# Kernel tuning notes

Hardware: AMD Instinct MI355X
Metric: run time of the kernel (lower is better)

## Reference

```python
import jax, jax.numpy as jnp
import numpy as np

N_NODES = 50000
N_EDGES = 1600000
IN_CH = 128
HID = 128
OUT_CH = 2
N_GRAPHS = 512
N_HID_LAYERS = 5  # first 5 SAGEConv+BN+ReLU blocks; 6th conv has no BN/act
EPS = 1e-5


def setup_inputs() -> dict:
    key = jax.random.key(0)
    ks = jax.random.split(key, 13)
    x = jax.random.normal(ks[0], (N_NODES, IN_CH), jnp.float32)
    edge_index = jax.random.randint(ks[1], (2, N_EDGES), 0, N_NODES)
    batch = jnp.sort(jax.random.randint(ks[2], (N_NODES,), 0, N_GRAPHS))
    s = 1.0 / np.sqrt(HID)
    # SAGEConv params for the 5 hidden layers (in==hid==128 so they stack)
    Wl = jax.random.normal(ks[3], (N_HID_LAYERS, HID, HID), jnp.float32) * s  # lin_l (neighbors)
    Wr = jax.random.normal(ks[4], (N_HID_LAYERS, HID, HID), jnp.float32) * s  # lin_r (root)
    b = jax.random.normal(ks[5], (N_HID_LAYERS, HID), jnp.float32) * s
    # BatchNorm (eval mode: running stats + affine)
    gamma = 1.0 + 0.1 * jax.random.normal(ks[6], (N_HID_LAYERS, HID), jnp.float32)
    beta = 0.1 * jax.random.normal(ks[7], (N_HID_LAYERS, HID), jnp.float32)
    rmean = 0.1 * jax.random.normal(ks[8], (N_HID_LAYERS, HID), jnp.float32)
    rvar = 0.5 + jax.random.uniform(ks[9], (N_HID_LAYERS, HID), dtype=jnp.float32)
    # final SAGEConv: hid -> out
    Wl_out = jax.random.normal(ks[10], (HID, OUT_CH), jnp.float32) * s
    Wr_out = jax.random.normal(ks[11], (HID, OUT_CH), jnp.float32) * s
    b_out = jax.random.normal(ks[12], (OUT_CH,), jnp.float32) * s
    return dict(x=x, Wl=Wl, Wr=Wr, b=b, gamma=gamma, beta=beta, rmean=rmean,
                rvar=rvar, Wl_out=Wl_out, Wr_out=Wr_out, b_out=b_out,
                edge_index=edge_index, batch=batch)


def reference(x, Wl, Wr, b, gamma, beta, rmean, rvar, Wl_out, Wr_out, b_out,
              edge_index, batch):
    src, dst = edge_index[0], edge_index[1]
    # in-degree for mean aggregation (shared across all layers)
    deg = jax.ops.segment_sum(jnp.ones((src.shape[0],), x.dtype), dst,
                              num_segments=N_NODES)
    inv_deg = (1.0 / jnp.maximum(deg, 1.0))[:, None]  # [N,1]

    def sage(h, Wl_, Wr_, b_):
        # PyG SAGEConv: lin_l(mean_{j in N(i)} x_j) + lin_r(x_i)
        agg = jax.ops.segment_sum(h[src], dst, num_segments=N_NODES) * inv_deg
        return agg @ Wl_ + h @ Wr_ + b_

    h = x
    for l in range(N_HID_LAYERS):
        h = sage(h, Wl[l], Wr[l], b[l])
        # BatchNorm1d in eval mode: affine with running stats
        h = (h - rmean[l]) * (gamma[l] * jax.lax.rsqrt(rvar[l] + EPS)) + beta[l]
        h = jax.nn.relu(h)
        # F.dropout(p=0.2, training=False) is identity in eval
    h = sage(h, Wl_out, Wr_out, b_out)  # [N, OUT_CH]
    # global_mean_pool over graphs
    gsum = jax.ops.segment_sum(h, batch, num_segments=N_GRAPHS)
    gcnt = jax.ops.segment_sum(jnp.ones((h.shape[0],), h.dtype), batch,
                               num_segments=N_GRAPHS)
    return gsum / jnp.maximum(gcnt, 1.0)[:, None]  # [N_GRAPHS, OUT_CH]
```

## Files before the change

### kernel.cpp

```cpp
#include <hip/hip_runtime.h>

#define HID 128
#define BN_EPS 1e-5f

typedef short bf16x8 __attribute__((ext_vector_type(8)));
typedef float f32x4 __attribute__((ext_vector_type(4)));

__device__ inline unsigned short f2b(float f) {
  unsigned int u = __float_as_uint(f);
  unsigned int r = (u + 0x7fffu + ((u >> 16) & 1u)) >> 16;
  return (unsigned short)r;
}
__device__ inline float bl(unsigned int v) { return __uint_as_float(v << 16); }
__device__ inline float bh(unsigned int v) { return __uint_as_float(v & 0xffff0000u); }


__global__ void k_bhist(const int* __restrict__ dst, int* __restrict__ bcnt, int e, int nb) {
  __shared__ int h[256];
  for (int i = threadIdx.x; i < 256; i += blockDim.x) h[i] = 0;
  __syncthreads();
  int stride = gridDim.x * blockDim.x;
  for (int i = blockIdx.x * blockDim.x + threadIdx.x; i < e; i += stride)
    atomicAdd(&h[dst[i] >> 8], 1);
  __syncthreads();
  for (int i = threadIdx.x; i < nb; i += blockDim.x)
    if (h[i]) atomicAdd(&bcnt[i], h[i]);
}

__global__ void k_bscan(const int* __restrict__ bcnt, int* __restrict__ base,
                        int* __restrict__ cur, int nb) {
  __shared__ int ws[4];
  int t = threadIdx.x;
  int v = (t < nb) ? bcnt[t] : 0;
  int lane = t & 63, wid = t >> 6;
  int x = v;
#pragma unroll
  for (int off = 1; off < 64; off <<= 1) {
    int y = __shfl_up(x, off, 64);
    if (lane >= off) x += y;
  }
  if (lane == 63) ws[wid] = x;
  __syncthreads();
  int add = 0;
  for (int w = 0; w < wid; ++w) add += ws[w];
  int incl = x + add;
  int excl = incl - v;
  if (t < nb) { base[t] = excl; cur[t] = excl; }
  if (t == nb - 1) base[nb] = incl;
}

__global__ void k_bscatter(const int* __restrict__ src, const int* __restrict__ dst,
                           int* __restrict__ cur, uint2* __restrict__ binned, int e) {
  __shared__ int bc[256];
  __shared__ int bo[256];
  int nchunk = (e + gridDim.x - 1) / gridDim.x;
  int c0 = blockIdx.x * nchunk;
  int c1 = min(c0 + nchunk, e);
  for (int i = threadIdx.x; i < 256; i += blockDim.x) bc[i] = 0;
  __syncthreads();
  for (int i = c0 + threadIdx.x; i < c1; i += blockDim.x)
    atomicAdd(&bc[dst[i] >> 8], 1);
  __syncthreads();
  for (int i = threadIdx.x; i < 256; i += blockDim.x) {
    int c = bc[i];
    bo[i] = c ? atomicAdd(&cur[i], c) : 0;
    bc[i] = 0;
  }
  __syncthreads();
  for (int i = c0 + threadIdx.x; i < c1; i += blockDim.x) {
    int d = dst[i];
    int b = d >> 8;
    int pos = bo[b] + atomicAdd(&bc[b], 1);
    binned[pos] = make_uint2((unsigned)src[i], (unsigned)d);
  }
}

__global__ __launch_bounds__(256) void k_bfill(
    const uint2* __restrict__ binned, const int* __restrict__ base,
    int* __restrict__ row_ptr, float* __restrict__ inv_deg,
    int* __restrict__ col, int n, int nb) {
  __shared__ int cnt[256];
  __shared__ int cur[256];
  __shared__ int ws[4];
  int b = blockIdx.x;
  int t = threadIdx.x;
  int n0 = b << 8;
  int e0 = base[b], e1 = base[b + 1];
  cnt[t] = 0;
  __syncthreads();
  for (int i = e0 + t; i < e1; i += 256)
    atomicAdd(&cnt[binned[i].y & 255], 1);
  __syncthreads();
  int v = cnt[t];
  int lane = t & 63, wid = t >> 6;
  int x = v;
#pragma unroll
  for (int off = 1; off < 64; off <<= 1) {
    int y = __shfl_up(x, off, 64);
    if (lane >= off) x += y;
  }
  if (lane == 63) ws[wid] = x;
  __syncthreads();
  int add = 0;
  for (int w = 0; w < wid; ++w) add += ws[w];
  int excl = x - v + add;
  int node = n0 + t;
  if (node < n) {
    row_ptr[node] = e0 + excl;
    inv_deg[node] = 1.0f / (float)max(v, 1);
  }
  cur[t] = e0 + excl;
  __syncthreads();
  for (int i = e0 + t; i < e1; i += 256) {
    uint2 pr = binned[i];
    int pos = atomicAdd(&cur[pr.y & 255], 1);
    col[pos] = (int)pr.x;
  }
  if (b == 0 && t == 0) row_ptr[n] = base[nb];
}


__global__ void k_prep(const float* __restrict__ x, unsigned short* __restrict__ xb,
                       const float* __restrict__ Wl, const float* __restrict__ Wr,
                       unsigned short* __restrict__ Wlt, unsigned short* __restrict__ Wrt,
                       const float* __restrict__ g, const float* __restrict__ be,
                       const float* __restrict__ rm, const float* __restrict__ rv,
                       float* __restrict__ sc, float* __restrict__ sh,
                       int n4, int wtot, int bn) {
  int i = blockIdx.x * blockDim.x + threadIdx.x;
  if (i < n4) {
    float4 v = ((const float4*)x)[i];
    unsigned int lo = (unsigned int)f2b(v.x) | ((unsigned int)f2b(v.y) << 16);
    unsigned int hi = (unsigned int)f2b(v.z) | ((unsigned int)f2b(v.w) << 16);
    ((uint2*)xb)[i] = make_uint2(lo, hi);
  } else if (i < n4 + wtot) {
    int j = i - n4;
    int mat = j >> 14, rem = j & 16383, nn = rem >> 7, kk = rem & 127;
    int sidx = (mat << 14) + (kk << 7) + nn;
    Wlt[j] = f2b(Wl[sidx]);
    Wrt[j] = f2b(Wr[sidx]);
  } else if (i < n4 + wtot + bn) {
    int j = i - n4 - wtot;
    float s = g[j] * rsqrtf(rv[j] + BN_EPS);
    sc[j] = s;
    sh[j] = be[j] - rm[j] * s;
  }
}


__global__ __launch_bounds__(256) void k_spmm_g(
    const unsigned short* __restrict__ hbsrc, const int* __restrict__ row_ptr,
    const int* __restrict__ col, const float* __restrict__ inv_deg,
    unsigned short* __restrict__ aggb, int n) {
  int node = blockIdx.x * 4 + (threadIdx.x >> 6);
  if (node >= n) return;
  int lane = threadIdx.x & 63;
  int slot = lane >> 4, c16 = lane & 15;
  int beg = row_ptr[node], end = row_ptr[node + 1];
  float a0 = 0, a1 = 0, a2 = 0, a3 = 0, a4 = 0, a5 = 0, a6 = 0, a7 = 0;
  const unsigned short* base = hbsrc + (c16 << 3);
  int e = beg;
  for (; e + 16 <= end; e += 16) {
    int s0 = col[e + slot];
    int s1 = col[e + 4 + slot];
    int s2 = col[e + 8 + slot];
    int s3 = col[e + 12 + slot];
    uint4 v0 = *(const uint4*)(base + ((size_t)s0 << 7));
    uint4 v1 = *(const uint4*)(base + ((size_t)s1 << 7));
    uint4 v2 = *(const uint4*)(base + ((size_t)s2 << 7));
    uint4 v3 = *(const uint4*)(base + ((size_t)s3 << 7));
    a0 += bl(v0.x); a1 += bh(v0.x); a2 += bl(v0.y); a3 += bh(v0.y);
    a4 += bl(v0.z); a5 += bh(v0.z); a6 += bl(v0.w); a7 += bh(v0.w);
    a0 += bl(v1.x); a1 += bh(v1.x); a2 += bl(v1.y); a3 += bh(v1.y);
    a4 += bl(v1.z); a5 += bh(v1.z); a6 += bl(v1.w); a7 += bh(v1.w);
    a0 += bl(v2.x); a1 += bh(v2.x); a2 += bl(v2.y); a3 += bh(v2.y);
    a4 += bl(v2.z); a5 += bh(v2.z); a6 += bl(v2.w); a7 += bh(v2.w);
    a0 += bl(v3.x); a1 += bh(v3.x); a2 += bl(v3.y); a3 += bh(v3.y);
    a4 += bl(v3.z); a5 += bh(v3.z); a6 += bl(v3.w); a7 += bh(v3.w);
  }
  for (; e < end; e += 4) {
    int idx = e + slot;
    if (idx < end) {
      int s = col[idx];
      uint4 v = *(const uint4*)(base + ((size_t)s << 7));
      a0 += bl(v.x); a1 += bh(v.x); a2 += bl(v.y); a3 += bh(v.y);
      a4 += bl(v.z); a5 += bh(v.z); a6 += bl(v.w); a7 += bh(v.w);
    }
  }
#pragma unroll
  for (int st = 16; st <= 32; st <<= 1) {
    a0 += __shfl_xor(a0, st); a1 += __shfl_xor(a1, st);
    a2 += __shfl_xor(a2, st); a3 += __shfl_xor(a3, st);
    a4 += __shfl_xor(a4, st); a5 += __shfl_xor(a5, st);
    a6 += __shfl_xor(a6, st); a7 += __shfl_xor(a7, st);
  }
  if (slot == 0) {
    float w = inv_deg[node];
    unsigned int p0 = (unsigned int)f2b(a0 * w) | ((unsigned int)f2b(a1 * w) << 16);
    unsigned int p1 = (unsigned int)f2b(a2 * w) | ((unsigned int)f2b(a3 * w) << 16);
    unsigned int p2 = (unsigned int)f2b(a4 * w) | ((unsigned int)f2b(a5 * w) << 16);
    unsigned int p3 = (unsigned int)f2b(a6 * w) | ((unsigned int)f2b(a7 * w) << 16);
    *(uint4*)(aggb + ((size_t)node << 7) + (c16 << 3)) = make_uint4(p0, p1, p2, p3);
  }
}


__global__ __launch_bounds__(256) void k_gemm3(
    const unsigned short* __restrict__ aggb,
    const unsigned short* __restrict__ hbsrc,
    const unsigned short* __restrict__ Wlt,
    const unsigned short* __restrict__ Wrt,
    const float* __restrict__ bias, const float* __restrict__ sc,
    const float* __restrict__ sh, unsigned short* __restrict__ hbo,
    int n, int ngroups) {
  int w = threadIdx.x >> 6;
  int lane = threadIdx.x & 63;
  int l15 = lane & 15, lhi = lane >> 4;

  bf16x8 aL[2][4], aR[2][4];
#pragma unroll
  for (int ms = 0; ms < 2; ++ms) {
    int row = (w << 5) + (ms << 4) + l15;
#pragma unroll
    for (int ks = 0; ks < 4; ++ks) {
      aL[ms][ks] = *(const bf16x8*)(Wlt + (row << 7) + (ks << 5) + (lhi << 3));
      aR[ms][ks] = *(const bf16x8*)(Wrt + (row << 7) + (ks << 5) + (lhi << 3));
    }
  }
  float4 bi[2], scv[2], shv[2];
#pragma unroll
  for (int ms = 0; ms < 2; ++ms) {
    int ch = (w << 5) + (ms << 4) + (lhi << 2);
    bi[ms] = *(const float4*)(bias + ch);
    scv[ms] = *(const float4*)(sc + ch);
    shv[ms] = *(const float4*)(sh + ch);
  }

  for (int g = blockIdx.x; g < ngroups; g += gridDim.x) {
    int node = (g << 4) + l15;
    bool ok = node < n;
    int nsafe = ok ? node : 0;
    const unsigned short* arow = aggb + ((size_t)nsafe << 7) + (lhi << 3);
    const unsigned short* hrow = hbsrc + ((size_t)nsafe << 7) + (lhi << 3);
    bf16x8 bA0 = *(const bf16x8*)(arow);
    bf16x8 bA1 = *(const bf16x8*)(arow + 32);
    bf16x8 bA2 = *(const bf16x8*)(arow + 64);
    bf16x8 bA3 = *(const bf16x8*)(arow + 96);
    bf16x8 bH0 = *(const bf16x8*)(hrow);
    bf16x8 bH1 = *(const bf16x8*)(hrow + 32);
    bf16x8 bH2 = *(const bf16x8*)(hrow + 64);
    bf16x8 bH3 = *(const bf16x8*)(hrow + 96);
    f32x4 acc[2];
#pragma unroll
    for (int ms = 0; ms < 2; ++ms) acc[ms] = (f32x4)(0.f);
#pragma unroll
    for (int ms = 0; ms < 2; ++ms) {
      acc[ms] = __builtin_amdgcn_mfma_f32_16x16x32_bf16(aL[ms][0], bA0, acc[ms], 0, 0, 0);
      acc[ms] = __builtin_amdgcn_mfma_f32_16x16x32_bf16(aL[ms][1], bA1, acc[ms], 0, 0, 0);
      acc[ms] = __builtin_amdgcn_mfma_f32_16x16x32_bf16(aL[ms][2], bA2, acc[ms], 0, 0, 0);
      acc[ms] = __builtin_amdgcn_mfma_f32_16x16x32_bf16(aL[ms][3], bA3, acc[ms], 0, 0, 0);
      acc[ms] = __builtin_amdgcn_mfma_f32_16x16x32_bf16(aR[ms][0], bH0, acc[ms], 0, 0, 0);
      acc[ms] = __builtin_amdgcn_mfma_f32_16x16x32_bf16(aR[ms][1], bH1, acc[ms], 0, 0, 0);
      acc[ms] = __builtin_amdgcn_mfma_f32_16x16x32_bf16(aR[ms][2], bH2, acc[ms], 0, 0, 0);
      acc[ms] = __builtin_amdgcn_mfma_f32_16x16x32_bf16(aR[ms][3], bH3, acc[ms], 0, 0, 0);
    }
    if (ok) {
#pragma unroll
      for (int ms = 0; ms < 2; ++ms) {
        int ch = (w << 5) + (ms << 4) + (lhi << 2);
        float o0 = fmaxf((acc[ms][0] + bi[ms].x) * scv[ms].x + shv[ms].x, 0.f);
        float o1 = fmaxf((acc[ms][1] + bi[ms].y) * scv[ms].y + shv[ms].y, 0.f);
        float o2 = fmaxf((acc[ms][2] + bi[ms].z) * scv[ms].z + shv[ms].z, 0.f);
        float o3 = fmaxf((acc[ms][3] + bi[ms].w) * scv[ms].w + shv[ms].w, 0.f);
        unsigned int lo = (unsigned int)f2b(o0) | ((unsigned int)f2b(o1) << 16);
        unsigned int hi = (unsigned int)f2b(o2) | ((unsigned int)f2b(o3) << 16);
        *(uint2*)(hbo + ((size_t)node << 7) + ch) = make_uint2(lo, hi);
      }
    }
  }
}


__global__ void k_pq(const unsigned short* __restrict__ hb, const float* __restrict__ Wl_out,
                     const float* __restrict__ Wr_out, float* __restrict__ p,
                     float* __restrict__ q, int n) {
  int node = blockIdx.x * 4 + (threadIdx.x >> 6);
  if (node >= n) return;
  int lane = threadIdx.x & 63;
  unsigned int hv = *(const unsigned int*)(hb + ((size_t)node << 7) + (lane << 1));
  float hx = bl(hv), hy = bh(hv);
  float4 wl = *(const float4*)(Wl_out + (lane << 2));
  float4 wr = *(const float4*)(Wr_out + (lane << 2));
  float p0 = hx * wl.x + hy * wl.z;
  float p1 = hx * wl.y + hy * wl.w;
  float q0 = hx * wr.x + hy * wr.z;
  float q1 = hx * wr.y + hy * wr.w;
#pragma unroll
  for (int off = 32; off > 0; off >>= 1) {
    p0 += __shfl_xor(p0, off, 64);
    p1 += __shfl_xor(p1, off, 64);
    q0 += __shfl_xor(q0, off, 64);
    q1 += __shfl_xor(q1, off, 64);
  }
  if (lane == 0) {
    *(float2*)(p + (size_t)node * 2) = make_float2(p0, p1);
    *(float2*)(q + (size_t)node * 2) = make_float2(q0, q1);
  }
}

__global__ void k_spmm2p(const float* __restrict__ p, const float* __restrict__ q,
                         const int* __restrict__ row_ptr, const int* __restrict__ col,
                         const float* __restrict__ inv_deg, const float* __restrict__ b_out,
                         const int* __restrict__ batch, float* __restrict__ out,
                         float* __restrict__ gcnt, int n) {
  int i = blockIdx.x * blockDim.x + threadIdx.x;
  int lane = threadIdx.x & 63;
  bool valid = i < n;
  float o0 = 0.f, o1 = 0.f;
  int g = -1;
  if (valid) {
    int beg = row_ptr[i], end = row_ptr[i + 1];
    float a0 = 0.f, a1 = 0.f, b0 = 0.f, b1 = 0.f;
    int e = beg;
    for (; e + 2 <= end; e += 2) {
      float2 v0 = *(const float2*)(p + (size_t)col[e] * 2);
      float2 v1 = *(const float2*)(p + (size_t)col[e + 1] * 2);
      a0 += v0.x; a1 += v0.y; b0 += v1.x; b1 += v1.y;
    }
    if (e < end) {
      float2 v = *(const float2*)(p + (size_t)col[e] * 2);
      a0 += v.x; a1 += v.y;
    }
    float w = inv_deg[i];
    float2 qv = *(const float2*)(q + (size_t)i * 2);
    o0 = (a0 + b0) * w + qv.x + b_out[0];
    o1 = (a1 + b1) * w + qv.y + b_out[1];
    g = batch[i];
  }
  float s0 = o0, s1 = o1;
#pragma unroll
  for (int off = 1; off < 64; off <<= 1) {
    float y0 = __shfl_up(s0, off, 64);
    float y1 = __shfl_up(s1, off, 64);
    if (lane >= off) { s0 += y0; s1 += y1; }
  }
  int gprev = __shfl_up(g, 1, 64);
  int gnext = __shfl_down(g, 1, 64);
  bool is_start = (lane == 0) || (g != gprev);
  bool is_end = valid && ((lane == 63) || (g != gnext));
  int startl = is_start ? lane : 0;
#pragma unroll
  for (int off = 1; off < 64; off <<= 1) {
    int y = __shfl_up(startl, off, 64);
    if (lane >= off) startl = max(startl, y);
  }
  int prevl = startl > 0 ? startl - 1 : 0;
  float t0 = __shfl(s0, prevl, 64);
  float t1 = __shfl(s1, prevl, 64);
  if (is_end) {
    float p0 = startl > 0 ? t0 : 0.f;
    float p1 = startl > 0 ? t1 : 0.f;
    atomicAdd(&out[g * 2], s0 - p0);
    atomicAdd(&out[g * 2 + 1], s1 - p1);
    atomicAdd(&gcnt[g], (float)(lane - startl + 1));
  }
}

__global__ void k_div(float* __restrict__ out, const float* __restrict__ gcnt, int ng) {
  int i = blockIdx.x * blockDim.x + threadIdx.x;
  if (i < ng * 2) out[i] /= fmaxf(gcnt[i >> 1], 1.0f);
}


extern "C" void kernel_launch(void* const* d_in, const int* in_sizes, int n_in,
                              void* d_out, int out_size, void* d_ws, size_t ws_size,
                              hipStream_t stream) {
  const float* x = (const float*)d_in[0];
  const float* Wl = (const float*)d_in[1];
  const float* Wr = (const float*)d_in[2];
  const float* b = (const float*)d_in[3];
  const float* gamma = (const float*)d_in[4];
  const float* beta = (const float*)d_in[5];
  const float* rmean = (const float*)d_in[6];
  const float* rvar = (const float*)d_in[7];
  const float* Wl_out = (const float*)d_in[8];
  const float* Wr_out = (const float*)d_in[9];
  const float* b_out = (const float*)d_in[10];
  const int* eidx = (const int*)d_in[11];
  const int* batch = (const int*)d_in[12];

  const int N = in_sizes[0] / HID;
  const int E = in_sizes[11] / 2;
  const int L = in_sizes[1] / (HID * HID);
  const int NG = out_size / 2;
  const int NB = (N + 255) >> 8;
  const int NGRP = (N + 15) >> 4;
  const int* src = eidx;
  const int* dst = eidx + E;

  char* ws = (char*)d_ws;
  size_t off = 0;
  auto alloc = [&](size_t bytes) {
    void* ptr = ws + off;
    off += (bytes + 255) & ~(size_t)255;
    return ptr;
  };
  int* row_ptr = (int*)alloc((size_t)(N + 1) * 4);
  int* bcnt = (int*)alloc((size_t)NB * 4);
  int* bbase = (int*)alloc((size_t)(NB + 1) * 4);
  int* bcur = (int*)alloc((size_t)NB * 4);
  int* col = (int*)alloc((size_t)E * 4);
  float* inv_deg = (float*)alloc((size_t)N * 4);
  unsigned short* xb = (unsigned short*)alloc((size_t)N * HID * 2);
  unsigned short* hb0 = (unsigned short*)alloc((size_t)N * HID * 2);
  unsigned short* hb1 = (unsigned short*)alloc((size_t)N * HID * 2);
  unsigned short* aggb = (unsigned short*)alloc((size_t)N * HID * 2);
  unsigned short* Wlt = (unsigned short*)alloc((size_t)L * HID * HID * 2);
  unsigned short* Wrt = (unsigned short*)alloc((size_t)L * HID * HID * 2);
  float* sc = (float*)alloc((size_t)L * HID * 4);
  float* sh = (float*)alloc((size_t)L * HID * 4);
  float* p = (float*)alloc((size_t)N * 2 * 4);
  float* q = (float*)alloc((size_t)N * 2 * 4);
  float* gcnt = (float*)alloc((size_t)NG * 4);
  uint2* binned = (uint2*)alloc((size_t)E * 8);

  hipMemsetAsync(bcnt, 0, (size_t)NB * 4, stream);
  k_bhist<<<256, 256, 0, stream>>>(dst, bcnt, E, NB);
  k_bscan<<<1, 256, 0, stream>>>(bcnt, bbase, bcur, NB);
  k_bscatter<<<256, 256, 0, stream>>>(src, dst, bcur, binned, E);
  k_bfill<<<NB, 256, 0, stream>>>(binned, bbase, row_ptr, inv_deg, col, N, NB);

  const int n4 = N * HID / 4;
  const int wtot = L * HID * HID;
  const int bn = L * HID;
  k_prep<<<(n4 + wtot + bn + 255) / 256, 256, 0, stream>>>(
      x, xb, Wl, Wr, Wlt, Wrt, gamma, beta, rmean, rvar, sc, sh, n4, wtot, bn);

  const unsigned short* hin = xb;
  for (int l = 0; l < L; ++l) {
    unsigned short* hnext = (l & 1) ? hb1 : hb0;
    k_spmm_g<<<(N + 3) / 4, 256, 0, stream>>>(hin, row_ptr, col, inv_deg, aggb, N);
    k_gemm3<<<512, 256, 0, stream>>>(
        aggb, hin, Wlt + (size_t)l * HID * HID, Wrt + (size_t)l * HID * HID,
        b + (size_t)l * HID, sc + (size_t)l * HID, sh + (size_t)l * HID,
        hnext, N, NGRP);
    hin = hnext;
  }
  k_pq<<<(N + 3) / 4, 256, 0, stream>>>(hin, Wl_out, Wr_out, p, q, N);
  hipMemsetAsync(d_out, 0, (size_t)out_size * 4, stream);
  hipMemsetAsync(gcnt, 0, (size_t)NG * 4, stream);
  k_spmm2p<<<(N + 255) / 256, 256, 0, stream>>>(
      p, q, row_ptr, col, inv_deg, b_out, batch, (float*)d_out, gcnt, N);
  k_div<<<(NG * 2 + 255) / 256, 256, 0, stream>>>((float*)d_out, gcnt, NG);
}
```

Baseline: 446.2 us.

## Process two nodes per wave in SpMM and GEMM, pack binned edges to 32-bit

The SpMM gather kernel now has each wavefront aggregate two destination nodes at once, interleaving their 16-edge gather batches so more independent loads are in flight and half as many blocks are launched. The fused GEMM processes two 16-node groups per iteration with separate accumulators, increasing MFMA and load-level parallelism. Edge binning packs the source index and the low destination bits into one 32-bit word, halving the binned buffer traffic. Storing the source in 16 bits caps node ids at 65535, which holds for 50000 nodes but breaks for larger graphs, and the extra accumulators raise register pressure.

```diff
diff --git a/kernel.cpp b/kernel.cpp
--- a/kernel.cpp
+++ b/kernel.cpp
@@ -50,7 +50,7 @@
 }
 
 __global__ void k_bscatter(const int* __restrict__ src, const int* __restrict__ dst,
-                           int* __restrict__ cur, uint2* __restrict__ binned, int e) {
+                           int* __restrict__ cur, unsigned int* __restrict__ binned, int e) {
   __shared__ int bc[256];
   __shared__ int bo[256];
   int nchunk = (e + gridDim.x - 1) / gridDim.x;
@@ -71,12 +71,12 @@
     int d = dst[i];
     int b = d >> 8;
     int pos = bo[b] + atomicAdd(&bc[b], 1);
-    binned[pos] = make_uint2((unsigned)src[i], (unsigned)d);
+    binned[pos] = (unsigned)src[i] | ((unsigned)(d & 255) << 16);
   }
 }
 
 __global__ __launch_bounds__(256) void k_bfill(
-    const uint2* __restrict__ binned, const int* __restrict__ base,
+    const unsigned int* __restrict__ binned, const int* __restrict__ base,
     int* __restrict__ row_ptr, float* __restrict__ inv_deg,
     int* __restrict__ col, int n, int nb) {
   __shared__ int cnt[256];
@@ -89,7 +89,7 @@
   cnt[t] = 0;
   __syncthreads();
   for (int i = e0 + t; i < e1; i += 256)
-    atomicAdd(&cnt[binned[i].y & 255], 1);
+    atomicAdd(&cnt[binned[i] >> 16], 1);
   __syncthreads();
   int v = cnt[t];
   int lane = t & 63, wid = t >> 6;
@@ -112,9 +112,9 @@
   cur[t] = e0 + excl;
   __syncthreads();
   for (int i = e0 + t; i < e1; i += 256) {
-    uint2 pr = binned[i];
-    int pos = atomicAdd(&cur[pr.y & 255], 1);
-    col[pos] = (int)pr.x;
+    unsigned int pr = binned[i];
+    int pos = atomicAdd(&cur[pr >> 16], 1);
+    col[pos] = (int)(pr & 0xffffu);
   }
   if (b == 0 && t == 0) row_ptr[n] = base[nb];
 }
@@ -148,59 +148,93 @@
 }
 
 
+#define GATHER16(EP, COLP, A)                                         \
+  {                                                                   \
+    int s0 = COLP[EP + slot];                                         \
+    int s1 = COLP[EP + 4 + slot];                                     \
+    int s2 = COLP[EP + 8 + slot];                                     \
+    int s3 = COLP[EP + 12 + slot];                                    \
+    uint4 v0 = *(const uint4*)(base + ((size_t)s0 << 7));             \
+    uint4 v1 = *(const uint4*)(base + ((size_t)s1 << 7));             \
+    uint4 v2 = *(const uint4*)(base + ((size_t)s2 << 7));             \
+    uint4 v3 = *(const uint4*)(base + ((size_t)s3 << 7));             \
+    A[0] += bl(v0.x); A[1] += bh(v0.x); A[2] += bl(v0.y); A[3] += bh(v0.y); \
+    A[4] += bl(v0.z); A[5] += bh(v0.z); A[6] += bl(v0.w); A[7] += bh(v0.w); \
+    A[0] += bl(v1.x); A[1] += bh(v1.x); A[2] += bl(v1.y); A[3] += bh(v1.y); \
+    A[4] += bl(v1.z); A[5] += bh(v1.z); A[6] += bl(v1.w); A[7] += bh(v1.w); \
+    A[0] += bl(v2.x); A[1] += bh(v2.x); A[2] += bl(v2.y); A[3] += bh(v2.y); \
+    A[4] += bl(v2.z); A[5] += bh(v2.z); A[6] += bl(v2.w); A[7] += bh(v2.w); \
+    A[0] += bl(v3.x); A[1] += bh(v3.x); A[2] += bl(v3.y); A[3] += bh(v3.y); \
+    A[4] += bl(v3.z); A[5] += bh(v3.z); A[6] += bl(v3.w); A[7] += bh(v3.w); \
+  }
+
 __global__ __launch_bounds__(256) void k_spmm_g(
     const unsigned short* __restrict__ hbsrc, const int* __restrict__ row_ptr,
     const int* __restrict__ col, const float* __restrict__ inv_deg,
     unsigned short* __restrict__ aggb, int n) {
-  int node = blockIdx.x * 4 + (threadIdx.x >> 6);
-  if (node >= n) return;
+  int na = blockIdx.x * 8 + ((threadIdx.x >> 6) << 1);
+  if (na >= n) return;
+  int nb_ = na + 1;
+  bool hasB = nb_ < n;
   int lane = threadIdx.x & 63;
   int slot = lane >> 4, c16 = lane & 15;
-  int beg = row_ptr[node], end = row_ptr[node + 1];
-  float a0 = 0, a1 = 0, a2 = 0, a3 = 0, a4 = 0, a5 = 0, a6 = 0, a7 = 0;
   const unsigned short* base = hbsrc + (c16 << 3);
-  int e = beg;
-  for (; e + 16 <= end; e += 16) {
-    int s0 = col[e + slot];
-    int s1 = col[e + 4 + slot];
-    int s2 = col[e + 8 + slot];
-    int s3 = col[e + 12 + slot];
-    uint4 v0 = *(const uint4*)(base + ((size_t)s0 << 7));
-    uint4 v1 = *(const uint4*)(base + ((size_t)s1 << 7));
-    uint4 v2 = *(const uint4*)(base + ((size_t)s2 << 7));
-    uint4 v3 = *(const uint4*)(base + ((size_t)s3 << 7));
-    a0 += bl(v0.x); a1 += bh(v0.x); a2 += bl(v0.y); a3 += bh(v0.y);
-    a4 += bl(v0.z); a5 += bh(v0.z); a6 += bl(v0.w); a7 += bh(v0.w);
-    a0 += bl(v1.x); a1 += bh(v1.x); a2 += bl(v1.y); a3 += bh(v1.y);
-    a4 += bl(v1.z); a5 += bh(v1.z); a6 += bl(v1.w); a7 += bh(v1.w);
-    a0 += bl(v2.x); a1 += bh(v2.x); a2 += bl(v2.y); a3 += bh(v2.y);
-    a4 += bl(v2.z); a5 += bh(v2.z); a6 += bl(v2.w); a7 += bh(v2.w);
-    a0 += bl(v3.x); a1 += bh(v3.x); a2 += bl(v3.y); a3 += bh(v3.y);
-    a4 += bl(v3.z); a5 += bh(v3.z); a6 += bl(v3.w); a7 += bh(v3.w);
-  }
-  for (; e < end; e += 4) {
-    int idx = e + slot;
-    if (idx < end) {
+
+  int ea = row_ptr[na], enda = row_ptr[na + 1];
+  int eb = hasB ? enda : 0;
+  int endb = hasB ? row_ptr[nb_ + 1] : 0;
+
+  float aA[8] = {0, 0, 0, 0, 0, 0, 0, 0};
+  float aB[8] = {0, 0, 0, 0, 0, 0, 0, 0};
+
+  while (ea + 16 <= enda && eb + 16 <= endb) {
+    GATHER16(ea, col, aA);
+    GATHER16(eb, col, aB);
+    ea += 16; eb += 16;
+  }
+  while (ea + 16 <= enda) { GATHER16(ea, col, aA); ea += 16; }
+  while (eb + 16 <= endb) { GATHER16(eb, col, aB); eb += 16; }
+  for (; ea < enda; ea += 4) {
+    int idx = ea + slot;
+    if (idx < enda) {
       int s = col[idx];
       uint4 v = *(const uint4*)(base + ((size_t)s << 7));
-      a0 += bl(v.x); a1 += bh(v.x); a2 += bl(v.y); a3 += bh(v.y);
-      a4 += bl(v.z); a5 += bh(v.z); a6 += bl(v.w); a7 += bh(v.w);
-    }
-  }
+      aA[0] += bl(v.x); aA[1] += bh(v.x); aA[2] += bl(v.y); aA[3] += bh(v.y);
+      aA[4] += bl(v.z); aA[5] += bh(v.z); aA[6] += bl(v.w); aA[7] += bh(v.w);
+    }
+  }
+  for (; eb < endb; eb += 4) {
+    int idx = eb + slot;
+    if (idx < endb) {
+      int s = col[idx];
+      uint4 v = *(const uint4*)(base + ((size_t)s << 7));
+      aB[0] += bl(v.x); aB[1] += bh(v.x); aB[2] += bl(v.y); aB[3] += bh(v.y);
+      aB[4] += bl(v.z); aB[5] += bh(v.z); aB[6] += bl(v.w); aB[7] += bh(v.w);
+    }
+  }
+
 #pragma unroll
   for (int st = 16; st <= 32; st <<= 1) {
-    a0 += __shfl_xor(a0, st); a1 += __shfl_xor(a1, st);
-    a2 += __shfl_xor(a2, st); a3 += __shfl_xor(a3, st);
-    a4 += __shfl_xor(a4, st); a5 += __shfl_xor(a5, st);
-    a6 += __shfl_xor(a6, st); a7 += __shfl_xor(a7, st);
+#pragma unroll
+    for (int j = 0; j < 8; ++j) {
+      aA[j] += __shfl_xor(aA[j], st);
+      aB[j] += __shfl_xor(aB[j], st);
+    }
   }
   if (slot == 0) {
-    float w = inv_deg[node];
-    unsigned int p0 = (unsigned int)f2b(a0 * w) | ((unsigned int)f2b(a1 * w) << 16);
-    unsigned int p1 = (unsigned int)f2b(a2 * w) | ((unsigned int)f2b(a3 * w) << 16);
-    unsigned int p2 = (unsigned int)f2b(a4 * w) | ((unsigned int)f2b(a5 * w) << 16);
-    unsigned int p3 = (unsigned int)f2b(a6 * w) | ((unsigned int)f2b(a7 * w) << 16);
-    *(uint4*)(aggb + ((size_t)node << 7) + (c16 << 3)) = make_uint4(p0, p1, p2, p3);
+    float w = inv_deg[na];
+    unsigned int p0 = (unsigned int)f2b(aA[0] * w) | ((unsigned int)f2b(aA[1] * w) << 16);
+    unsigned int p1 = (unsigned int)f2b(aA[2] * w) | ((unsigned int)f2b(aA[3] * w) << 16);
+    unsigned int p2 = (unsigned int)f2b(aA[4] * w) | ((unsigned int)f2b(aA[5] * w) << 16);
+    unsigned int p3 = (unsigned int)f2b(aA[6] * w) | ((unsigned int)f2b(aA[7] * w) << 16);
+    *(uint4*)(aggb + ((size_t)na << 7) + (c16 << 3)) = make_uint4(p0, p1, p2, p3);
+  } else if (slot == 1 && hasB) {
+    float w = inv_deg[nb_];
+    unsigned int p0 = (unsigned int)f2b(aB[0] * w) | ((unsigned int)f2b(aB[1] * w) << 16);
+    unsigned int p1 = (unsigned int)f2b(aB[2] * w) | ((unsigned int)f2b(aB[3] * w) << 16);
+    unsigned int p2 = (unsigned int)f2b(aB[4] * w) | ((unsigned int)f2b(aB[5] * w) << 16);
+    unsigned int p3 = (unsigned int)f2b(aB[6] * w) | ((unsigned int)f2b(aB[7] * w) << 16);
+    *(uint4*)(aggb + ((size_t)nb_ << 7) + (c16 << 3)) = make_uint4(p0, p1, p2, p3);
   }
 }
 
@@ -236,45 +270,63 @@
     shv[ms] = *(const float4*)(sh + ch);
   }
 
-  for (int g = blockIdx.x; g < ngroups; g += gridDim.x) {
-    int node = (g << 4) + l15;
-    bool ok = node < n;
-    int nsafe = ok ? node : 0;
-    const unsigned short* arow = aggb + ((size_t)nsafe << 7) + (lhi << 3);
-    const unsigned short* hrow = hbsrc + ((size_t)nsafe << 7) + (lhi << 3);
-    bf16x8 bA0 = *(const bf16x8*)(arow);
-    bf16x8 bA1 = *(const bf16x8*)(arow + 32);
-    bf16x8 bA2 = *(const bf16x8*)(arow + 64);
-    bf16x8 bA3 = *(const bf16x8*)(arow + 96);
-    bf16x8 bH0 = *(const bf16x8*)(hrow);
-    bf16x8 bH1 = *(const bf16x8*)(hrow + 32);
-    bf16x8 bH2 = *(const bf16x8*)(hrow + 64);
-    bf16x8 bH3 = *(const bf16x8*)(hrow + 96);
-    f32x4 acc[2];
-#pragma unroll
-    for (int ms = 0; ms < 2; ++ms) acc[ms] = (f32x4)(0.f);
+  for (int g0 = blockIdx.x * 2; g0 < ngroups; g0 += gridDim.x * 2) {
+    int g1 = g0 + 1;
+    int nodeA = (g0 << 4) + l15;
+    bool okA = nodeA < n;
+    bool okB = (g1 < ngroups);
+    int nodeB = okB ? (g1 << 4) + l15 : nodeA;
+    okB = okB && nodeB < n;
+    int nsA = okA ? nodeA : 0;
+    int nsB = okB ? nodeB : 0;
+    const unsigned short* arowA = aggb + ((size_t)nsA << 7) + (lhi << 3);
+    const unsigned short* hrowA = hbsrc + ((size_t)nsA << 7) + (lhi << 3);
+    const unsigned short* arowB = aggb + ((size_t)nsB << 7) + (lhi << 3);
+    const unsigned short* hrowB = hbsrc + ((size_t)nsB << 7) + (lhi << 3);
+    bf16x8 bA[4], bH[4], cA[4], cH[4];
+#pragma unroll
+    for (int ks = 0; ks < 4; ++ks) {
+      bA[ks] = *(const bf16x8*)(arowA + (ks << 5));
+      bH[ks] = *(const bf16x8*)(hrowA + (ks << 5));
+      cA[ks] = *(const bf16x8*)(arowB + (ks << 5));
+      cH[ks] = *(const bf16x8*)(hrowB + (ks << 5));
+    }
+    f32x4 acc0[2], acc1[2];
+#pragma unroll
+    for (int ms = 0; ms < 2; ++ms) { acc0[ms] = (f32x4)(0.f); acc1[ms] = (f32x4)(0.f); }
 #pragma unroll
     for (int ms = 0; ms < 2; ++ms) {
-      acc[ms] = __builtin_amdgcn_mfma_f32_16x16x32_bf16(aL[ms][0], bA0, acc[ms], 0, 0, 0);
-      acc[ms] = __builtin_amdgcn_mfma_f32_16x16x32_bf16(aL[ms][1], bA1, acc[ms], 0, 0, 0);
-      acc[ms] = __builtin_amdgcn_mfma_f32_16x16x32_bf16(aL[ms][2], bA2, acc[ms], 0, 0, 0);
-      acc[ms] = __builtin_amdgcn_mfma_f32_16x16x32_bf16(aL[ms][3], bA3, acc[ms], 0, 0, 0);
-      acc[ms] = __builtin_amdgcn_mfma_f32_16x16x32_bf16(aR[ms][0], bH0, acc[ms], 0, 0, 0);
-      acc[ms] = __builtin_amdgcn_mfma_f32_16x16x32_bf16(aR[ms][1], bH1, acc[ms], 0, 0, 0);
-      acc[ms] = __builtin_amdgcn_mfma_f32_16x16x32_bf16(aR[ms][2], bH2, acc[ms], 0, 0, 0);
-      acc[ms] = __builtin_amdgcn_mfma_f32_16x16x32_bf16(aR[ms][3], bH3, acc[ms], 0, 0, 0);
-    }
-    if (ok) {
-#pragma unroll
-      for (int ms = 0; ms < 2; ++ms) {
-        int ch = (w << 5) + (ms << 4) + (lhi << 2);
-        float o0 = fmaxf((acc[ms][0] + bi[ms].x) * scv[ms].x + shv[ms].x, 0.f);
-        float o1 = fmaxf((acc[ms][1] + bi[ms].y) * scv[ms].y + shv[ms].y, 0.f);
-        float o2 = fmaxf((acc[ms][2] + bi[ms].z) * scv[ms].z + shv[ms].z, 0.f);
-        float o3 = fmaxf((acc[ms][3] + bi[ms].w) * scv[ms].w + shv[ms].w, 0.f);
+#pragma unroll
+      for (int ks = 0; ks < 4; ++ks) {
+        acc0[ms] = __builtin_amdgcn_mfma_f32_16x16x32_bf16(aL[ms][ks], bA[ks], acc0[ms], 0, 0, 0);
+        acc1[ms] = __builtin_amdgcn_mfma_f32_16x16x32_bf16(aL[ms][ks], cA[ks], acc1[ms], 0, 0, 0);
+      }
+#pragma unroll
+      for (int ks = 0; ks < 4; ++ks) {
+        acc0[ms] = __builtin_amdgcn_mfma_f32_16x16x32_bf16(aR[ms][ks], bH[ks], acc0[ms], 0, 0, 0);
+        acc1[ms] = __builtin_amdgcn_mfma_f32_16x16x32_bf16(aR[ms][ks], cH[ks], acc1[ms], 0, 0, 0);
+      }
+    }
+#pragma unroll
+    for (int ms = 0; ms < 2; ++ms) {
+      int ch = (w << 5) + (ms << 4) + (lhi << 2);
+      if (okA) {
+        float o0 = fmaxf((acc0[ms][0] + bi[ms].x) * scv[ms].x + shv[ms].x, 0.f);
+        float o1 = fmaxf((acc0[ms][1] + bi[ms].y) * scv[ms].y + shv[ms].y, 0.f);
+        float o2 = fmaxf((acc0[ms][2] + bi[ms].z) * scv[ms].z + shv[ms].z, 0.f);
+        float o3 = fmaxf((acc0[ms][3] + bi[ms].w) * scv[ms].w + shv[ms].w, 0.f);
         unsigned int lo = (unsigned int)f2b(o0) | ((unsigned int)f2b(o1) << 16);
         unsigned int hi = (unsigned int)f2b(o2) | ((unsigned int)f2b(o3) << 16);
-        *(uint2*)(hbo + ((size_t)node << 7) + ch) = make_uint2(lo, hi);
+        *(uint2*)(hbo + ((size_t)nodeA << 7) + ch) = make_uint2(lo, hi);
+      }
+      if (okB) {
+        float o0 = fmaxf((acc1[ms][0] + bi[ms].x) * scv[ms].x + shv[ms].x, 0.f);
+        float o1 = fmaxf((acc1[ms][1] + bi[ms].y) * scv[ms].y + shv[ms].y, 0.f);
+        float o2 = fmaxf((acc1[ms][2] + bi[ms].z) * scv[ms].z + shv[ms].z, 0.f);
+        float o3 = fmaxf((acc1[ms][3] + bi[ms].w) * scv[ms].w + shv[ms].w, 0.f);
+        unsigned int lo = (unsigned int)f2b(o0) | ((unsigned int)f2b(o1) << 16);
+        unsigned int hi = (unsigned int)f2b(o2) | ((unsigned int)f2b(o3) << 16);
+        *(uint2*)(hbo + ((size_t)nodeB << 7) + ch) = make_uint2(lo, hi);
       }
     }
   }
@@ -422,7 +474,7 @@
   float* p = (float*)alloc((size_t)N * 2 * 4);
   float* q = (float*)alloc((size_t)N * 2 * 4);
   float* gcnt = (float*)alloc((size_t)NG * 4);
-  uint2* binned = (uint2*)alloc((size_t)E * 8);
+  unsigned int* binned = (unsigned int*)alloc((size_t)E * 4);
 
   hipMemsetAsync(bcnt, 0, (size_t)NB * 4, stream);
   k_bhist<<<256, 256, 0, stream>>>(dst, bcnt, E, NB);
@@ -439,7 +491,7 @@
   const unsigned short* hin = xb;
   for (int l = 0; l < L; ++l) {
     unsigned short* hnext = (l & 1) ? hb1 : hb0;
-    k_spmm_g<<<(N + 3) / 4, 256, 0, stream>>>(hin, row_ptr, col, inv_deg, aggb, N);
+    k_spmm_g<<<(N + 7) / 8, 256, 0, stream>>>(hin, row_ptr, col, inv_deg, aggb, N);
     k_gemm3<<<512, 256, 0, stream>>>(
         aggb, hin, Wlt + (size_t)l * HID * HID, Wrt + (size_t)l * HID * HID,
         b + (size_t)l * HID, sc + (size_t)l * HID, sh + (size_t)l * HID,
```

Measured after the change: 482.2 us. 1.08x slower.
